# Performance work log

Hardware: AMD Instinct MI355X
Metric: run time of the kernel (lower is better)

Reference implementation:

```python
import jax, jax.numpy as jnp
import numpy as np


def _flip_roll(a):
    # torch.roll(torch.flip(a, [-3,-2,-1]), (1,1,1), [-3,-2,-1])
    return jnp.roll(jnp.flip(a, axis=(-3, -2, -1)), shift=(1, 1, 1), axis=(-3, -2, -1))


def dht_3d(x):
    dims = (2, 3, 4)
    r = jnp.fft.fftn(x, axes=dims).real - jnp.fft.fftn(jnp.flip(x, axis=-1), axes=dims).imag
    norm = jnp.sqrt(jnp.sum(r * r, axis=dims, keepdims=True))
    safe = jnp.where(norm == 0, 1.0, norm)
    return jnp.where(norm != 0, r / safe, jnp.zeros_like(r))


def compl_mul3d(x1, x2):
    x1n = _flip_roll(x1)
    x2n = _flip_roll(x2)
    return 0.5 * (
        jnp.einsum('bixyz,ioxyz->boxyz', x1, x2)
        - jnp.einsum('bixyz,ioxyz->boxyz', x1n, x2n)
        + jnp.einsum('bixyz,ioxyz->boxyz', x1, x2n)
        + jnp.einsum('bixyz,ioxyz->boxyz', x1n, x2)
    )


def idht_3d(X):
    n = X.shape[2] * X.shape[3] * X.shape[4]
    return dht_3d(X) / n


def setup_inputs() -> dict:
    key = jax.random.key(0)
    k1, k2 = jax.random.split(key)
    B, Cin, Cout = 4, 32, 32
    S = 64
    M = 8
    scale = 1.0 / (Cin * Cout)
    x = jax.random.normal(k1, (B, Cin, S, S, S), dtype=jnp.float32)
    weights1 = scale * jax.random.uniform(k2, (Cin, Cout, M, M, M), dtype=jnp.float32)
    return {"x": x, "weights1": weights1}


def reference(x, weights1):
    B = x.shape[0]
    Cout = weights1.shape[1]
    m1, m2, m3 = weights1.shape[2], weights1.shape[3], weights1.shape[4]
    s1, s2, s3 = x.shape[-3], x.shape[-2], x.shape[-1]
    x_ht = dht_3d(x)
    conv = compl_mul3d(x_ht[:, :, :m1, :m2, :m3], weights1)
    out_ht = jnp.zeros((B, Cout, s1, s2, s3), dtype=x.dtype)
    out_ht = out_ht.at[:, :, :m1, :m2, :m3].set(conv)
    return idht_3d(out_ht)
```

## Files before the change

kernel.cpp:

```cpp
#include <hip/hip_runtime.h>
#include <math.h>


constexpr int NT = 262144;
constexpr float TWOPI_64 = 0.09817477042468103f;


__global__ __launch_bounds__(256) void k_fwd1(const float* __restrict__ x,
                                              float* __restrict__ S,
                                              float* __restrict__ red1p) {
  __shared__ float As[64 * 68];
  __shared__ float Bs[64 * 68];
  __shared__ float PL[32 * 65];
  __shared__ float tw1[1024];
  __shared__ float rsm[12];
  const int t = threadIdx.x;
  const int j = blockIdx.x;
  const int bc = blockIdx.y;
  const int n1a = j, n1b = (64 - j) & 63;
  const bool paired = (n1a != n1b);
  for (int u = t; u < 1024; u += 256) {
    int n3 = u >> 4, k3q = (u >> 2) & 3, jj = u & 3;
    int k3 = k3q + ((jj >> 1) << 2);
    float ang = TWOPI_64 * (float)((k3 * n3) & 63);
    tw1[u] = (jj & 1) ? sinf(ang) : cosf(ang);
  }
  const float4* xa4 = (const float4*)(x + ((size_t)bc << 18) + (n1a << 12));
  const float4* xb4 = (const float4*)(x + ((size_t)bc << 18) + (n1b << 12));
  float ssp = 0.f;
  for (int q = 0; q < 4; ++q) {
    int l4 = t + (q << 8);
    int fl = l4 << 2;
    int r = fl >> 6, c = fl & 63;
    float4 va = xa4[l4], vb = xb4[l4];
    *(float4*)&As[r * 68 + c] = va;
    *(float4*)&Bs[r * 68 + c] = vb;
    ssp += va.x * va.x + va.y * va.y + va.z * va.z + va.w * va.w;
    if (paired) ssp += vb.x * vb.x + vb.y * vb.y + vb.z * vb.z + vb.w * vb.w;
  }
  __syncthreads();
  const int n2 = t & 63;
  const int k3q = t >> 6;
  {
    float reA0 = 0, imA0 = 0, reA1 = 0, imA1 = 0;
    float reB0 = 0, imB0 = 0, reB1 = 0, imB1 = 0;
    const float4* Ar = (const float4*)&As[n2 * 68];
    const float4* Br = (const float4*)&Bs[n2 * 68];
    const float4* T4 = (const float4*)tw1;
    for (int m = 0; m < 16; ++m) {
      float4 va = Ar[m], vb = Br[m];
      float av[4] = {va.x, va.y, va.z, va.w};
      float bv[4] = {vb.x, vb.y, vb.z, vb.w};
#pragma unroll
      for (int e = 0; e < 4; ++e) {
        float4 tw = T4[(m << 4) + (e << 2) + k3q];
        float a = av[e], b = bv[e];
        reA0 += a * tw.x; imA0 -= a * tw.y;
        reB0 += b * tw.x; imB0 -= b * tw.y;
        reA1 += a * tw.z; imA1 -= a * tw.w;
        reB1 += b * tw.z; imB1 -= b * tw.w;
      }
    }
    PL[(k3q) * 65 + n2] = reA0;       PL[(8 + k3q) * 65 + n2] = imA0;
    PL[(16 + k3q) * 65 + n2] = reB0;  PL[(24 + k3q) * 65 + n2] = imB0;
    PL[(4 + k3q) * 65 + n2] = reA1;   PL[(12 + k3q) * 65 + n2] = imA1;
    PL[(20 + k3q) * 65 + n2] = reB1;  PL[(28 + k3q) * 65 + n2] = imB1;
  }
  float c1p = 0.f, c2p = 0.f;
  for (int q = 0; q < 16; ++q) {
    int l = t + (q << 8);
    int r = l >> 6, c = l & 63;
    float a = As[r * 68 + c];
    int m2 = (64 - r) & 63;
    int m3 = (64 - c) & 63;
    int m3b = (62 - c) & 63;
    c1p += a * Bs[m2 * 68 + m3];
    c2p += a * Bs[m2 * 68 + m3b];
  }
  if (paired) { c1p *= 2.f; c2p *= 2.f; }
  for (int off = 32; off; off >>= 1) {
    ssp += __shfl_down(ssp, off);
    c1p += __shfl_down(c1p, off);
    c2p += __shfl_down(c2p, off);
  }
  const int lane = t & 63, wid = t >> 6;
  if (lane == 0) { rsm[wid * 3] = ssp; rsm[wid * 3 + 1] = c1p; rsm[wid * 3 + 2] = c2p; }
  __syncthreads();
  if (t == 0) {
    red1p[((size_t)bc * 33 + j) * 3 + 0] = rsm[0] + rsm[3] + rsm[6] + rsm[9];
    red1p[((size_t)bc * 33 + j) * 3 + 1] = rsm[1] + rsm[4] + rsm[7] + rsm[10];
    red1p[((size_t)bc * 33 + j) * 3 + 2] = rsm[2] + rsm[5] + rsm[8] + rsm[11];
  }
  {
    const int k2 = t & 7;
    const int rr = t >> 3;
    const int row = rr >> 4, f = (rr >> 3) & 1, k3 = rr & 7;
    float re = 0.f, im = 0.f;
    const float* pr = &PL[rr * 65];
    const int tb = ((k2 & 3) << 2) + ((k2 >> 2) << 1);
#pragma unroll 4
    for (int n2i = 0; n2i < 64; ++n2i) {
      float v = pr[n2i];
      const float2 cs = *(const float2*)&tw1[(n2i << 4) + tb];
      re += v * cs.x; im -= v * cs.y;
    }
    const int n1row = row ? n1b : n1a;
    ((float2*)S)[(((size_t)bc * 64 + n1row) * 2 + f) * 64 + k2 * 8 + k3] =
        make_float2(re, im);
  }
}

__global__ __launch_bounds__(256) void k_fwd2s(const float* __restrict__ S,
                                               const float* __restrict__ red1p,
                                               float* __restrict__ xh) {
  __shared__ float2 U3L[256];
  __shared__ float2 tw[8 * 66];
  __shared__ float rbuf[99];
  const int t = threadIdx.x;
  const int h = blockIdx.x;
  const int bc = blockIdx.y;
  for (int u = t; u < 512; u += 256) {
    int k1 = u >> 6, n1 = u & 63;
    float ang = TWOPI_64 * (float)((k1 * n1) & 63);
    tw[k1 * 66 + n1] = make_float2(cosf(ang), sinf(ang));
  }
  if (t < 99) rbuf[t] = red1p[(size_t)bc * 99 + t];
  __syncthreads();
  {
    const int kkl = t & 15;
    const int f = (t >> 4) & 1;
    const int k1 = t >> 5;
    const int rr2 = f * 64 + h * 16 + kkl;
    const float2* Sb = (const float2*)(S + ((size_t)bc << 14));
    const float2* tk = &tw[k1 * 66];
    float re = 0.f, im = 0.f;
#pragma unroll 4
    for (int n1 = 0; n1 < 64; ++n1) {
      float2 ab = Sb[(n1 << 7) + rr2];
      float2 cs = tk[n1];
      re += ab.x * cs.x + ab.y * cs.y;
      im += ab.y * cs.x - ab.x * cs.y;
    }
    U3L[f * 128 + k1 * 16 + kkl] = make_float2(re, im);
  }
  __syncthreads();
  float ss = 0.f, c1 = 0.f, c2 = 0.f;
  for (int jj = 0; jj < 33; ++jj) {
    ss += rbuf[jj * 3];
    c1 += rbuf[jj * 3 + 1];
    c2 += rbuf[jj * 3 + 2];
  }
  float nsq = 0.5f * (float)NT * (2.f * ss + c1 - c2);
  float inv1 = nsq > 0.f ? rsqrtf(nsq) : 0.f;
  if (t < 128) {
    const int k1 = t >> 4, kkl = t & 15;
    const int kk = h * 16 + kkl;
    const int k3 = kk & 7;
    float2 U = U3L[k1 * 16 + kkl];
    float2 V = U3L[128 + k1 * 16 + kkl];
    float2 cs = tw[k3 * 66 + 1];
    float r = U.x - V.y - cs.y * (U.x + V.y) - cs.x * (U.y - V.x);
    xh[(size_t)bc * 512 + k1 * 64 + kk] = r * inv1;
  }
}

__global__ __launch_bounds__(256) void k_mixA(const float* __restrict__ xh,
                                              const float* __restrict__ w,
                                              float* __restrict__ A1,
                                              float* __restrict__ inv2q) {
  __shared__ float xsh[16384];
  __shared__ float convL[8 * 33];
  __shared__ float c64v[64], s64v[64];
  __shared__ float psum[4];
  const int t = threadIdx.x;
  const int bh = blockIdx.x;
  const int h = bh & 1;
  const int bc2 = bh >> 1;
  const int b = bc2 >> 5, o = bc2 & 31;
  if (t < 64) { float ang = TWOPI_64 * t; c64v[t] = cosf(ang); s64v[t] = sinf(ang); }
  const float4* xb4 = (const float4*)(xh + ((size_t)b << 14));
  float4* xs4 = (float4*)xsh;
  for (int q = 0; q < 16; ++q) xs4[t + (q << 8)] = xb4[t + (q << 8)];
  __syncthreads();
  const int n1m = t >> 5;
  const int col32 = t & 31;
  const int col = (h << 5) + col32;
  const int n2 = col >> 3, n3 = col & 7;
  const int k = (n1m << 6) + col;
  const int nk = (((8 - n1m) & 7) << 6) + (((8 - n2) & 7) << 3) + ((8 - n3) & 7);
  float acc = 0.f;
  const float* wb = w + ((size_t)o << 9);
#pragma unroll 4
  for (int i = 0; i < 32; ++i) {
    const float* wr = wb + ((size_t)i << 14);
    float xa = xsh[(i << 9) + k], xn = xsh[(i << 9) + nk];
    acc += (xa + xn) * wr[k] + (xa - xn) * wr[nk];
  }
  const float cval = 0.5f * acc;
  convL[n1m * 33 + col32] = cval;
  float p = cval * cval;
  for (int off = 32; off; off >>= 1) p += __shfl_down(p, off);
  if ((t & 63) == 0) psum[t >> 6] = p;
  __syncthreads();
  if (t == 0) {
    float Q = 2.f * (psum[0] + psum[1] + psum[2] + psum[3]);
    if (h == 0) { float c000 = convL[0]; Q += c000 * c000; }
    inv2q[bc2 * 2 + h] = Q;
  }
  const int q8 = t >> 5;
  float cv[8];
#pragma unroll
  for (int n1i = 0; n1i < 8; ++n1i) cv[n1i] = convL[n1i * 33 + col32];
  float2* A1p = (float2*)(A1 + ((size_t)bc2 << 13));
  for (int it = 0; it < 8; ++it) {
    const int k1 = q8 + (it << 3);
    float re = 0.f, im = 0.f;
#pragma unroll
    for (int n1i = 0; n1i < 8; ++n1i) {
      int a = (k1 * n1i) & 63;
      re += cv[n1i] * c64v[a];
      im -= cv[n1i] * s64v[a];
    }
    A1p[(k1 << 6) + col] = make_float2(re, im);
  }
}

__global__ __launch_bounds__(256) void k_expBC(const float* __restrict__ A1,
                                               const float* __restrict__ inv2q,
                                               float* __restrict__ out) {
  __shared__ float arow[128];
  __shared__ float B2[64 * 20];
  __shared__ float c64v[64], s64v[64];
  const int t = threadIdx.x;
  const int k1 = blockIdx.x;
  const int bc2 = blockIdx.y;
  const float q0 = inv2q[bc2 * 2], q1 = inv2q[bc2 * 2 + 1];
  if (t < 64) { float ang = TWOPI_64 * t; c64v[t] = cosf(ang); s64v[t] = sinf(ang); }
  if (t < 128) arow[t] = A1[((size_t)bc2 << 13) + (k1 << 7) + t];
  __syncthreads();
  {
    const int k2 = t & 63;
    const int g = t >> 6;
    const int f = g & 1;
    const int n3h = (g >> 1) << 2;
    float acc[4] = {0, 0, 0, 0};
    for (int n2i = 0; n2i < 8; ++n2i) {
      int a_ = (k2 * n2i) & 63;
      float tc = c64v[a_], ts = s64v[a_];
      const float4* ar4 = (const float4*)&arow[((n2i << 3) + n3h) << 1];
      float4 p0 = ar4[0];
      float4 p1 = ar4[1];
      if (f == 0) {
        acc[0] += p0.x * tc + p0.y * ts;
        acc[1] += p0.z * tc + p0.w * ts;
        acc[2] += p1.x * tc + p1.y * ts;
        acc[3] += p1.z * tc + p1.w * ts;
      } else {
        acc[0] += p0.y * tc - p0.x * ts;
        acc[1] += p0.w * tc - p0.z * ts;
        acc[2] += p1.y * tc - p1.x * ts;
        acc[3] += p1.w * tc - p1.z * ts;
      }
    }
    *(float4*)&B2[k2 * 20 + (f << 3) + n3h] = make_float4(acc[0], acc[1], acc[2], acc[3]);
  }
  __syncthreads();
  {
    const int k3 = t & 63;
    const int wid = t >> 6;
    float C1r[8], C2r[8];
#pragma unroll
    for (int n3 = 0; n3 < 8; ++n3) {
      int a0 = (k3 * n3) & 63;
      int a1 = (k3 * (n3 + 1)) & 63;
      C1r[n3] = c64v[a0] - s64v[a1];
      C2r[n3] = s64v[a0] - c64v[a1];
    }
    float nsq = 0.5f * (float)NT * (q0 + q1);
    const float sc = nsq > 0.f ? 1.f / (sqrtf(nsq) * (float)NT) : 0.f;
    float* dst = out + ((size_t)bc2 << 18) + (k1 << 12);
    for (int it = 0; it < 16; ++it) {
      int k2 = (wid << 4) + it;
      const float4* br4 = (const float4*)&B2[k2 * 20];
      float4 r0 = br4[0], r1 = br4[1], r2 = br4[2], r3 = br4[3];
      float acc = r0.x * C1r[0] + r0.y * C1r[1] + r0.z * C1r[2] + r0.w * C1r[3]
                + r1.x * C1r[4] + r1.y * C1r[5] + r1.z * C1r[6] + r1.w * C1r[7]
                + r2.x * C2r[0] + r2.y * C2r[1] + r2.z * C2r[2] + r2.w * C2r[3]
                + r3.x * C2r[4] + r3.y * C2r[5] + r3.z * C2r[6] + r3.w * C2r[7];
      dst[(k2 << 6) + k3] = acc * sc;
    }
  }
}

extern "C" void kernel_launch(void* const* d_in, const int* in_sizes, int n_in,
                              void* d_out, int out_size, void* d_ws, size_t ws_size,
                              hipStream_t stream) {
  const float* x = (const float*)d_in[0];
  const float* w = (const float*)d_in[1];
  float* out = (float*)d_out;
  float* ws = (float*)d_ws;
  float* S     = ws;
  float* red1p = ws + 2097152;
  float* xh    = ws + 2109824;
  float* inv2q = ws + 2175360;
  float* A1    = ws + 2175616;

  k_fwd1 <<<dim3(33, 128), 256, 0, stream>>>(x, S, red1p);
  k_fwd2s<<<dim3(4, 128),  256, 0, stream>>>(S, red1p, xh);
  k_mixA <<<dim3(256),     256, 0, stream>>>(xh, w, A1, inv2q);
  k_expBC<<<dim3(64, 128), 256, 0, stream>>>(A1, inv2q, out);
}
```

Baseline: 271.3 us.

## Restructure final expansion kernel: contract n3 first, precomputed k2 twiddle table

The output expansion kernel now contracts the n3 dimension first into per-n2 P/Q registers and then expands over k2 using a global twiddle table precomputed by the first kernel. Each block handles four k1 rows (one per wavefront), so the grid shrinks fourfold and the intermediate shared-memory stage and second barrier go away. The twiddle loads use a wave-uniform index to encourage scalar loads. Correctness now depends on k_fwd1 block (0,0) writing the table before k_expBC runs, which the stream order guarantees.

```diff
diff --git a/kernel.cpp b/kernel.cpp
--- a/kernel.cpp
+++ b/kernel.cpp
@@ -8,7 +8,8 @@
 
 __global__ __launch_bounds__(256) void k_fwd1(const float* __restrict__ x,
                                               float* __restrict__ S,
-                                              float* __restrict__ red1p) {
+                                              float* __restrict__ red1p,
+                                              float* __restrict__ TB2g) {
   __shared__ float As[64 * 68];
   __shared__ float Bs[64 * 68];
   __shared__ float PL[32 * 65];
@@ -19,9 +20,16 @@
   const int bc = blockIdx.y;
   const int n1a = j, n1b = (64 - j) & 63;
   const bool paired = (n1a != n1b);
+  if (j == 0 && bc == 0) {
+    for (int u = t; u < 1024; u += 256) {
+      int k2 = u >> 4, i = u & 15, n2 = i >> 1;
+      float ang = TWOPI_64 * (float)((k2 * n2) & 63);
+      TB2g[u] = (i & 1) ? sinf(ang) : cosf(ang);
+    }
+  }
   for (int u = t; u < 1024; u += 256) {
-    int n3 = u >> 4, k3q = (u >> 2) & 3, jj = u & 3;
-    int k3 = k3q + ((jj >> 1) << 2);
+    int n3 = u >> 4, k3q_ = (u >> 2) & 3, jj = u & 3;
+    int k3 = k3q_ + ((jj >> 1) << 2);
     float ang = TWOPI_64 * (float)((k3 * n3) & 63);
     tw1[u] = (jj & 1) ? sinf(ang) : cosf(ang);
   }
@@ -227,68 +235,62 @@
 
 __global__ __launch_bounds__(256) void k_expBC(const float* __restrict__ A1,
                                                const float* __restrict__ inv2q,
+                                               const float* __restrict__ TB2g,
                                                float* __restrict__ out) {
-  __shared__ float arow[128];
-  __shared__ float B2[64 * 20];
+  __shared__ float arows[512];
   __shared__ float c64v[64], s64v[64];
   const int t = threadIdx.x;
-  const int k1 = blockIdx.x;
+  const int k1g = blockIdx.x;
   const int bc2 = blockIdx.y;
-  const float q0 = inv2q[bc2 * 2], q1 = inv2q[bc2 * 2 + 1];
+  const int wid = t >> 6, lane = t & 63;
   if (t < 64) { float ang = TWOPI_64 * t; c64v[t] = cosf(ang); s64v[t] = sinf(ang); }
-  if (t < 128) arow[t] = A1[((size_t)bc2 << 13) + (k1 << 7) + t];
-  __syncthreads();
-  {
-    const int k2 = t & 63;
-    const int g = t >> 6;
-    const int f = g & 1;
-    const int n3h = (g >> 1) << 2;
-    float acc[4] = {0, 0, 0, 0};
-    for (int n2i = 0; n2i < 8; ++n2i) {
-      int a_ = (k2 * n2i) & 63;
-      float tc = c64v[a_], ts = s64v[a_];
-      const float4* ar4 = (const float4*)&arow[((n2i << 3) + n3h) << 1];
-      float4 p0 = ar4[0];
-      float4 p1 = ar4[1];
-      if (f == 0) {
-        acc[0] += p0.x * tc + p0.y * ts;
-        acc[1] += p0.z * tc + p0.w * ts;
-        acc[2] += p1.x * tc + p1.y * ts;
-        acc[3] += p1.z * tc + p1.w * ts;
-      } else {
-        acc[0] += p0.y * tc - p0.x * ts;
-        acc[1] += p0.w * tc - p0.z * ts;
-        acc[2] += p1.y * tc - p1.x * ts;
-        acc[3] += p1.w * tc - p1.z * ts;
-      }
-    }
-    *(float4*)&B2[k2 * 20 + (f << 3) + n3h] = make_float4(acc[0], acc[1], acc[2], acc[3]);
-  }
-  __syncthreads();
-  {
-    const int k3 = t & 63;
-    const int wid = t >> 6;
-    float C1r[8], C2r[8];
-#pragma unroll
-    for (int n3 = 0; n3 < 8; ++n3) {
-      int a0 = (k3 * n3) & 63;
-      int a1 = (k3 * (n3 + 1)) & 63;
-      C1r[n3] = c64v[a0] - s64v[a1];
-      C2r[n3] = s64v[a0] - c64v[a1];
-    }
-    float nsq = 0.5f * (float)NT * (q0 + q1);
-    const float sc = nsq > 0.f ? 1.f / (sqrtf(nsq) * (float)NT) : 0.f;
-    float* dst = out + ((size_t)bc2 << 18) + (k1 << 12);
-    for (int it = 0; it < 16; ++it) {
-      int k2 = (wid << 4) + it;
-      const float4* br4 = (const float4*)&B2[k2 * 20];
-      float4 r0 = br4[0], r1 = br4[1], r2 = br4[2], r3 = br4[3];
-      float acc = r0.x * C1r[0] + r0.y * C1r[1] + r0.z * C1r[2] + r0.w * C1r[3]
-                + r1.x * C1r[4] + r1.y * C1r[5] + r1.z * C1r[6] + r1.w * C1r[7]
-                + r2.x * C2r[0] + r2.y * C2r[1] + r2.z * C2r[2] + r2.w * C2r[3]
-                + r3.x * C2r[4] + r3.y * C2r[5] + r3.z * C2r[6] + r3.w * C2r[7];
-      dst[(k2 << 6) + k3] = acc * sc;
-    }
+  if (t < 128) {
+    const float4* src = (const float4*)(A1 + ((size_t)bc2 << 13) + (k1g << 9));
+    ((float4*)arows)[t] = src[t];
+  }
+  __syncthreads();
+  float C1r[8], C2r[8];
+#pragma unroll
+  for (int n3 = 0; n3 < 8; ++n3) {
+    int a0 = (lane * n3) & 63;
+    int a1 = (lane * (n3 + 1)) & 63;
+    C1r[n3] = c64v[a0] - s64v[a1];
+    C2r[n3] = s64v[a0] - c64v[a1];
+  }
+  float P[8], Q[8];
+  const float4* Ar = (const float4*)&arows[wid << 7];
+#pragma unroll
+  for (int n2 = 0; n2 < 8; ++n2) {
+    float4 q0 = Ar[n2 * 4 + 0];
+    float4 q1 = Ar[n2 * 4 + 1];
+    float4 q2 = Ar[n2 * 4 + 2];
+    float4 q3 = Ar[n2 * 4 + 3];
+    float p = 0.f, qq = 0.f;
+    p  += q0.x * C1r[0] + q0.y * C2r[0] + q0.z * C1r[1] + q0.w * C2r[1];
+    qq += q0.y * C1r[0] - q0.x * C2r[0] + q0.w * C1r[1] - q0.z * C2r[1];
+    p  += q1.x * C1r[2] + q1.y * C2r[2] + q1.z * C1r[3] + q1.w * C2r[3];
+    qq += q1.y * C1r[2] - q1.x * C2r[2] + q1.w * C1r[3] - q1.z * C2r[3];
+    p  += q2.x * C1r[4] + q2.y * C2r[4] + q2.z * C1r[5] + q2.w * C2r[5];
+    qq += q2.y * C1r[4] - q2.x * C2r[4] + q2.w * C1r[5] - q2.z * C2r[5];
+    p  += q3.x * C1r[6] + q3.y * C2r[6] + q3.z * C1r[7] + q3.w * C2r[7];
+    qq += q3.y * C1r[6] - q3.x * C2r[6] + q3.w * C1r[7] - q3.z * C2r[7];
+    P[n2] = p; Q[n2] = qq;
+  }
+  const float q0v = inv2q[bc2 * 2], q1v = inv2q[bc2 * 2 + 1];
+  const float nsq = 0.5f * (float)NT * (q0v + q1v);
+  const float sc = nsq > 0.f ? 1.f / (sqrtf(nsq) * (float)NT) : 0.f;
+  const int k1 = (k1g << 2) + wid;
+  float* dst = out + ((size_t)bc2 << 18) + (k1 << 12);
+#pragma unroll 4
+  for (int k2 = 0; k2 < 64; ++k2) {
+    const int k2u = __builtin_amdgcn_readfirstlane(k2);
+    const float4* TBk = (const float4*)(TB2g + (k2u << 4));
+    float4 t0 = TBk[0], t1 = TBk[1], t2 = TBk[2], t3 = TBk[3];
+    float acc = t0.x * P[0] + t0.y * Q[0] + t0.z * P[1] + t0.w * Q[1]
+              + t1.x * P[2] + t1.y * Q[2] + t1.z * P[3] + t1.w * Q[3]
+              + t2.x * P[4] + t2.y * Q[4] + t2.z * P[5] + t2.w * Q[5]
+              + t3.x * P[6] + t3.y * Q[6] + t3.z * P[7] + t3.w * Q[7];
+    dst[(k2 << 6) + lane] = acc * sc;
   }
 }
 
@@ -304,9 +306,10 @@
   float* xh    = ws + 2109824;
   float* inv2q = ws + 2175360;
   float* A1    = ws + 2175616;
-
-  k_fwd1 <<<dim3(33, 128), 256, 0, stream>>>(x, S, red1p);
+  float* TB2g  = ws + 3224192;
+
+  k_fwd1 <<<dim3(33, 128), 256, 0, stream>>>(x, S, red1p, TB2g);
   k_fwd2s<<<dim3(4, 128),  256, 0, stream>>>(S, red1p, xh);
   k_mixA <<<dim3(256),     256, 0, stream>>>(xh, w, A1, inv2q);
-  k_expBC<<<dim3(64, 128), 256, 0, stream>>>(A1, inv2q, out);
-}
+  k_expBC<<<dim3(16, 128), 256, 0, stream>>>(A1, inv2q, TB2g, out);
+}
```

New measurement: 285.3 us. 5.2% more time.
